# Kernel optimization log

Hardware: AMD Instinct MI355X
Metric: run time of the kernel (lower is better)

## Reference

```python
import jax, jax.numpy as jnp
import numpy as np

IMG = 1280
STRIDES = (8, 16, 32)
ALPHA, GAMMA = 0.25, 2.0
OBJ_W, BOX_W, FOOT_W = 1.0, 5.0, 1.0
RADIUS, NUM_CAND, EPS = 2.5, 10, 1e-7


def _grid(H, W):
    ys, xs = jnp.meshgrid(jnp.arange(H, dtype=jnp.float32),
                          jnp.arange(W, dtype=jnp.float32), indexing='ij')
    return xs.reshape(-1), ys.reshape(-1)


def _iou_xyxy(a, b):
    lt = jnp.maximum(a[..., :2], b[..., :2])
    rb = jnp.minimum(a[..., 2:], b[..., 2:])
    wh = jnp.clip(rb - lt, 0.0)
    inter = wh[..., 0] * wh[..., 1]
    aa = (a[..., 2] - a[..., 0]) * (a[..., 3] - a[..., 1])
    ab = (b[..., 2] - b[..., 0]) * (b[..., 3] - b[..., 1])
    return inter / (aa + ab - inter + EPS)


def _assign_one(pred, gt_boxes, gt_foots, gt_valid, stride):
    # Faithful SimOTAAssigner.assign for one image/scale (torch @no_grad).
    pred = jax.lax.stop_gradient(pred)
    gt_boxes = jax.lax.stop_gradient(gt_boxes)
    gt_foots = jax.lax.stop_gradient(gt_foots)
    C, H, W = pred.shape
    HW = H * W
    gx, gy = _grid(H, W)
    s = stride / IMG
    p = pred.reshape(C, HW)
    obj_logit = p[0]
    pcx = (jax.nn.sigmoid(p[1]) + gx) * s
    pcy = (jax.nn.sigmoid(p[2]) + gy) * s
    pw = jnp.exp(jnp.clip(p[3], -5.0, 5.0)) * s
    ph = jnp.exp(jnp.clip(p[4], -5.0, 5.0)) * s
    pred_xyxy = jnp.stack([pcx - pw / 2, pcy - ph / 2, pcx + pw / 2, pcy + ph / 2], -1)
    cls_cost = jax.nn.softplus(-obj_logit)  # BCE_with_logits(logit, 1)
    cell = jnp.arange(HW)

    def step(carry, gt):
        obj_t, box_t, foot_t, pos_m = carry
        box, foot, valid = gt
        cx, cy, w, h = box[0], box[1], box[2], box[3]
        cxg, cyg = cx / s, cy / s
        in_center = (jnp.abs(gx - cxg) < RADIUS) & (jnp.abs(gy - cyg) < RADIUS)
        in_box = ((gx >= (cx - w / 2) / s) & (gx < (cx + w / 2) / s) &
                  (gy >= (cy - h / 2) / s) & (gy < (cy + h / 2) / s))
        cand = in_center | in_box
        dist = (gx - cxg) ** 2 + (gy - cyg) ** 2
        cand = jnp.where(jnp.any(cand), cand, cell == jnp.argmin(dist))
        gt_xyxy = jnp.stack([cx - w / 2, cy - h / 2, cx + w / 2, cy + h / 2])
        iou = _iou_xyxy(pred_xyxy, gt_xyxy)  # (HW,)
        cost = jnp.where(cand, cls_cost - 3.0 * jnp.log(iou + EPS), jnp.inf)
        n_cand = jnp.sum(cand)
        iou_sum = jnp.sum(jnp.where(cand, iou, 0.0))
        n_pos = jnp.clip(jnp.floor(iou_sum).astype(jnp.int32), 1,
                         jnp.minimum(NUM_CAND, n_cand))
        _, idx = jax.lax.top_k(-cost, NUM_CAND)
        sel = (jnp.arange(NUM_CAND) < n_pos) & valid
        best_iou = iou[idx[0]]  # pair_iou[topk_idx[0]] in the torch code
        pos_m = pos_m.at[idx].max(sel.astype(jnp.float32))
        obj_t = obj_t.at[idx].max(jnp.where(sel, best_iou, -jnp.inf))
        tx = cxg - gx[idx]
        ty = cyg - gy[idx]
        tw = jnp.log(w / s + EPS)
        th = jnp.log(h / s + EPS)
        new_box = jnp.stack([tx, ty, jnp.full_like(tx, tw), jnp.full_like(tx, th)], 0)
        box_t = box_t.at[:, idx].set(jnp.where(sel, new_box, box_t[:, idx]))
        new_foot = jnp.stack([jnp.full_like(tx, foot[0]), jnp.full_like(tx, foot[1])], 0)
        foot_t = foot_t.at[:, idx].set(jnp.where(sel, new_foot, foot_t[:, idx]))
        return (obj_t, box_t, foot_t, pos_m), None

    init = (jnp.zeros(HW), jnp.zeros((4, HW)), jnp.zeros((2, HW)), jnp.zeros(HW))
    (obj_t, box_t, foot_t, pos_m), _ = jax.lax.scan(
        step, init, (gt_boxes, gt_foots, gt_valid))
    return obj_t, box_t, foot_t, pos_m


def _ciou(pcx, pcy, pw, ph, tcx, tcy, tw, th):
    px1, py1, px2, py2 = pcx - pw / 2, pcy - ph / 2, pcx + pw / 2, pcy + ph / 2
    tx1, ty1, tx2, ty2 = tcx - tw / 2, tcy - th / 2, tcx + tw / 2, tcy + th / 2
    iw = jnp.clip(jnp.minimum(px2, tx2) - jnp.maximum(px1, tx1), 0.0)
    ih = jnp.clip(jnp.minimum(py2, ty2) - jnp.maximum(py1, ty1), 0.0)
    inter = iw * ih
    union = pw * ph + tw * th - inter + EPS
    iou = inter / union
    rho2 = (pcx - tcx) ** 2 + (pcy - tcy) ** 2
    cw = jnp.maximum(px2, tx2) - jnp.minimum(px1, tx1)
    ch = jnp.maximum(py2, ty2) - jnp.minimum(py1, ty1)
    c2 = cw ** 2 + ch ** 2 + EPS
    v = (4.0 / jnp.pi ** 2) * (jnp.arctan(tw / (th + EPS)) - jnp.arctan(pw / (ph + EPS))) ** 2
    alpha = jax.lax.stop_gradient(v / (1.0 - iou + v + EPS))
    return iou - rho2 / c2 - alpha * v


def _loss_one(pred, gt_boxes, gt_foots, gt_valid, stride):
    obj_t, box_t, foot_t, pm = _assign_one(pred, gt_boxes, gt_foots, gt_valid, stride)
    C, H, W = pred.shape
    HW = H * W
    p = pred.reshape(C, HW)
    gx, gy = _grid(H, W)
    s = stride / IMG
    # focal loss on objectness with soft IoU targets
    x, z = p[0], obj_t
    ce = jnp.maximum(x, 0.0) - x * z + jnp.log1p(jnp.exp(-jnp.abs(x)))
    prob = jax.nn.sigmoid(x)
    p_t = prob * z + (1.0 - prob) * (1.0 - z)
    a_t = ALPHA * z + (1.0 - ALPHA) * (1.0 - z)
    obj_loss = jnp.mean(a_t * (1.0 - p_t) ** GAMMA * ce)
    npos = jnp.maximum(jnp.sum(pm), 1.0)
    # CIoU box loss at positive cells (mask instead of gather, jit-friendly)
    pcx = (jax.nn.sigmoid(p[1]) + gx) * s
    pcy = (jax.nn.sigmoid(p[2]) + gy) * s
    pw = jnp.exp(jnp.clip(p[3], -5.0, 5.0)) * s
    ph = jnp.exp(jnp.clip(p[4], -5.0, 5.0)) * s
    tcx = (box_t[0] + gx) * s
    tcy = (box_t[1] + gy) * s
    tw = jnp.exp(box_t[2]) * s
    th = jnp.exp(box_t[3]) * s
    ciou = _ciou(pcx, pcy, pw, ph, tcx, tcy, tw, th)
    box_loss = jnp.sum(pm * (1.0 - ciou)) / npos
    # smooth-L1 foot loss on sigmoid-decoded foot point
    pf = jax.nn.sigmoid(p[5:7])
    d = jnp.abs(pf - foot_t)
    sl1 = jnp.where(d < 1.0, 0.5 * d * d, d - 0.5)
    foot_loss = jnp.sum(pm * jnp.sum(sl1, 0)) / npos
    return obj_loss, box_loss, foot_loss


def _forward(pred_s0, pred_s1, pred_s2, targets):
    B = pred_s0.shape[0]
    person = targets[..., 0] == 0  # person_mask; padded rows use cls != 0
    boxes = targets[..., 1:5]
    foots = targets[..., 5:7]
    size = jnp.maximum(boxes[..., 2], boxes[..., 3]) * IMG
    scale_masks = (size < 128.0, (size >= 48.0) & (size < 288.0), size >= 128.0)
    tot_obj = tot_box = tot_foot = 0.0
    for pred, stride, sm in zip((pred_s0, pred_s1, pred_s2), STRIDES, scale_masks):
        valid = person & sm
        o, bx, f = jax.vmap(_loss_one, in_axes=(0, 0, 0, 0, None))(
            pred, boxes, foots, valid, stride)
        tot_obj = tot_obj + jnp.sum(o)
        tot_box = tot_box + jnp.sum(bx)
        tot_foot = tot_foot + jnp.sum(f)
    return (OBJ_W * tot_obj + BOX_W * tot_box + FOOT_W * tot_foot) / B


def setup_inputs() -> dict:
    key = jax.random.key(0)
    ks = jax.random.split(key, 7)
    B, N = 64, 40
    pred_s0 = jax.random.normal(ks[0], (B, 7, 160, 160), jnp.float32)
    pred_s1 = jax.random.normal(ks[1], (B, 7, 80, 80), jnp.float32)
    pred_s2 = jax.random.normal(ks[2], (B, 7, 40, 40), jnp.float32)
    cls = (jax.random.uniform(ks[3], (B, N, 1)) > 0.9).astype(jnp.float32)
    cxy = jax.random.uniform(ks[4], (B, N, 2)) * 0.8 + 0.1
    wh = jax.random.uniform(ks[5], (B, N, 2)) * 0.28 + 0.01
    ft = jax.random.uniform(ks[6], (B, N, 2))
    targets = jnp.concatenate([cls, cxy, wh, ft], -1)
    return {"pred_s0": pred_s0, "pred_s1": pred_s1, "pred_s2": pred_s2,
            "targets": targets}


def reference(pred_s0, pred_s1, pred_s2, targets):
    return _forward(pred_s0, pred_s1, pred_s2, targets)
```

## Files before the change

kernel.cpp:

```cpp
#include <hip/hip_runtime.h>
#include <math.h>

#define NBATCH 64
#define NGT    40
#define HW0    25600
#define HW1    6400
#define HW2    1600
#define NTASK  (NBATCH*3*NGT)
#define MAXE   400
#define SENT   0xFFFFFFFFFFFFFFFFull
#define FEPS   1e-7f

__device__ __forceinline__ float frcp(float x){ return __builtin_amdgcn_rcpf(x); }
__device__ __forceinline__ float fsigm(float x){ return frcp(1.0f + __expf(-x)); }
__device__ __forceinline__ float sigm(float x){ return 1.0f/(1.0f+expf(-x)); }

__device__ __forceinline__ float focal0(float x){
  float e = __expf(-fabsf(x));
  float ce = fmaxf(x,0.0f) + __logf(1.0f+e);
  float prob = fsigm(x);
  return 0.75f*prob*prob*ce;
}
__device__ __forceinline__ float focalz(float x, float z){
  float e = __expf(-fabsf(x));
  float ce = fmaxf(x,0.0f) - x*z + __logf(1.0f+e);
  float prob = fsigm(x);
  float p_t = prob*z + (1.0f-prob)*(1.0f-z);
  float a_t = 0.25f*z + 0.75f*(1.0f-z);
  float om = 1.0f-p_t;
  return a_t*om*om*ce;
}

__device__ __forceinline__ unsigned fkey(float f){
  unsigned b = __float_as_uint(f);
  return (b & 0x80000000u) ? ~b : (b | 0x80000000u);
}

__device__ __forceinline__ unsigned long long shflx64(unsigned long long v, int m){
  int lo = __shfl_xor((int)(unsigned)(v & 0xFFFFFFFFull), m, 64);
  int hi = __shfl_xor((int)(unsigned)(v >> 32), m, 64);
  return (((unsigned long long)(unsigned)hi) << 32) | (unsigned)lo;
}
__device__ __forceinline__ float wredf(float v){
  #pragma unroll
  for (int o=32;o;o>>=1) v += __shfl_xor(v,o,64);
  return v;
}
__device__ __forceinline__ int wredi(int v){
  #pragma unroll
  for (int o=32;o;o>>=1) v += __shfl_xor(v,o,64);
  return v;
}
__device__ __forceinline__ unsigned long long wredmin64(unsigned long long v){
  #pragma unroll
  for (int o=32;o;o>>=1){ unsigned long long w = shflx64(v,o); v = (w<v)?w:v; }
  return v;
}

__device__ __forceinline__ float iou_of_cell(const float* __restrict__ P, int HW, int cell,
                                             int W, float s,
                                             float bx1, float by1, float bx2, float by2, float ab){
  int gy = cell / W;
  int gx = cell - gy*W;
  float gxf=(float)gx, gyf=(float)gy;
  float q1 = P[HW+cell], q2=P[2*HW+cell], q3=P[3*HW+cell], q4=P[4*HW+cell];
  float pcx = (sigm(q1)+gxf)*s;
  float pcy = (sigm(q2)+gyf)*s;
  float pw = expf(fminf(fmaxf(q3,-5.0f),5.0f))*s;
  float ph = expf(fminf(fmaxf(q4,-5.0f),5.0f))*s;
  float ax1=pcx-pw*0.5f, ay1=pcy-ph*0.5f, ax2=pcx+pw*0.5f, ay2=pcy+ph*0.5f;
  float ltx=fmaxf(ax1,bx1), lty=fmaxf(ay1,by1);
  float rbx=fminf(ax2,bx2), rby=fminf(ay2,by2);
  float iw=fmaxf(rbx-ltx,0.0f), ih=fmaxf(rby-lty,0.0f);
  float inter=iw*ih;
  float aa=(ax2-ax1)*(ay2-ay1);
  return inter/(aa+ab-inter+FEPS);
}

__global__ __launch_bounds__(256) void k_assign(
    const float* __restrict__ p0, const float* __restrict__ p1,
    const float* __restrict__ p2, const float* __restrict__ tg,
    int2* __restrict__ meta, int* __restrict__ cells,
    float* __restrict__ out)
{
  if (blockIdx.x == 0 && threadIdx.x == 0) out[0] = 0.0f;
  int lane = threadIdx.x & 63;
  int task = ((blockIdx.x<<8) + threadIdx.x) >> 6;
  int g  = task % NGT;
  int bs = task / NGT;
  int sc = bs % 3;
  int b  = bs / 3;

  const float* tp = tg + (b*NGT + g)*7;
  float cls = tp[0], cx = tp[1], cy = tp[2], w = tp[3], h = tp[4];
  float sz = fmaxf(w,h)*1280.0f;
  bool valid = (cls == 0.0f);
  if (sc==0)      valid = valid && (sz < 128.0f);
  else if (sc==1) valid = valid && (sz >= 48.0f) && (sz < 288.0f);
  else            valid = valid && (sz >= 128.0f);
  if (!valid){ if (lane==0) meta[task] = make_int2(0,0); return; }

  int W, HW; float s; const float* P;
  if (sc==0)      { W=160; HW=HW0; s=8.0f/1280.0f;  P=p0; }
  else if (sc==1) { W=80;  HW=HW1; s=16.0f/1280.0f; P=p1; }
  else            { W=40;  HW=HW2; s=32.0f/1280.0f; P=p2; }
  P += (size_t)b*7*HW;

  float inv_s = 1280.0f/(float)((sc==0)?8:(sc==1)?16:32);
  float cxg = cx*inv_s, cyg = cy*inv_s;
  float bx1 = cx - w*0.5f, bx2 = cx + w*0.5f;
  float by1 = cy - h*0.5f, by2 = cy + h*0.5f;
  float ab  = (bx2-bx1)*(by2-by1);
  float bxl = bx1*inv_s, bxr = bx2*inv_s, byt = by1*inv_s, byb = by2*inv_s;

  int x0 = max(0,   (int)floorf(fminf(cxg-2.5f, bxl)) - 1);
  int x1 = min(W-1, (int)floorf(fmaxf(cxg+2.5f, bxr)) + 1);
  int y0 = max(0,   (int)floorf(fminf(cyg-2.5f, byt)) - 1);
  int y1 = min(W-1, (int)floorf(fmaxf(cyg+2.5f, byb)) + 1);
  int rw = x1-x0+1, rh = y1-y0+1;
  int rn = rw*rh;

  unsigned long long t[10];
  #pragma unroll
  for (int j=0;j<10;++j) t[j]=SENT;
  int ncand = 0; float iousum = 0.0f;
  unsigned long long dmin = SENT;

  int rx = lane % rw, ry = lane / rw;
  int stepy = 64 / rw, stepx = 64 % rw;
  for (int r = lane; r < rn; r += 64){
    float gxf = (float)(x0+rx), gyf = (float)(y0+ry);
    int cell = (y0+ry)*W + (x0+rx);
    float q1 = P[HW+cell], q2 = P[2*HW+cell], q3 = P[3*HW+cell], q4 = P[4*HW+cell];
    float pcx = (fsigm(q1)+gxf)*s;
    float pcy = (fsigm(q2)+gyf)*s;
    float pw = __expf(fminf(fmaxf(q3,-5.0f),5.0f))*s;
    float ph = __expf(fminf(fmaxf(q4,-5.0f),5.0f))*s;
    float ax1 = pcx-pw*0.5f, ay1 = pcy-ph*0.5f, ax2 = pcx+pw*0.5f, ay2 = pcy+ph*0.5f;
    float ltx = fmaxf(ax1,bx1), lty = fmaxf(ay1,by1);
    float rbx = fminf(ax2,bx2), rby = fminf(ay2,by2);
    float iw = fmaxf(rbx-ltx,0.0f), ih = fmaxf(rby-lty,0.0f);
    float inter = iw*ih;
    float aa = (ax2-ax1)*(ay2-ay1);
    float iou = inter * frcp(aa+ab-inter+FEPS);
    bool ic = (fabsf(gxf-cxg)<2.5f) && (fabsf(gyf-cyg)<2.5f);
    bool ib = (gxf>=bxl)&&(gxf<bxr)&&(gyf>=byt)&&(gyf<byb);
    float dx = gxf-cxg, dy = gyf-cyg;
    float dist = dx*dx+dy*dy;
    unsigned long long dk = (((unsigned long long)__float_as_uint(dist))<<32)|(unsigned)cell;
    dmin = (dk<dmin)?dk:dmin;
    if (ic|ib){
      ncand += 1; iousum += iou;
      float q0 = P[cell];
      float ccost = fmaxf(-q0,0.0f) + __logf(1.0f + __expf(-fabsf(q0)));
      float cost = ccost - 3.0f*__logf(iou+FEPS);
      unsigned long long pk = (((unsigned long long)fkey(cost))<<32)|(unsigned)cell;
      if (pk < t[9]){
        t[9] = pk;
        #pragma unroll
        for (int j=9;j>0;--j){ if (t[j]<t[j-1]){ unsigned long long tmp=t[j]; t[j]=t[j-1]; t[j-1]=tmp; } }
      }
    }
    rx += stepx; ry += stepy;
    if (rx >= rw){ rx -= rw; ry += 1; }
  }

  int NC = wredi(ncand);
  float IS = wredf(iousum);
  dmin = wredmin64(dmin);

  unsigned long long g10[10];
  int ptr = 0;
  #pragma unroll
  for (int rd=0; rd<10; ++rd){
    unsigned long long head = SENT;
    #pragma unroll
    for (int j=0;j<10;++j) head = (ptr==j)? t[j] : head;
    unsigned long long m = wredmin64(head);
    g10[rd] = m;
    if (head==m && m!=SENT) ptr += 1;
  }

  if (lane==0){
    unsigned cell0; int npos;
    if (NC==0){ cell0 = (unsigned)dmin; npos = 1; }
    else {
      cell0 = (unsigned)g10[0];
      int ub = NC < 10 ? NC : 10;
      int v = (int)floorf(IS);
      v = v < 1 ? 1 : v;
      npos = v > ub ? ub : v;
    }
    float biou = iou_of_cell(P, HW, (int)cell0, W, s, bx1, by1, bx2, by2, ab);
    meta[task] = make_int2(npos, __float_as_int(biou));
    #pragma unroll
    for (int sl=0; sl<10; ++sl){
      if (sl < npos) cells[task*10 + sl] = (int)((sl==0)? cell0 : (unsigned)g10[sl]);
    }
  }
}

__global__ __launch_bounds__(512) void k_pos(
    const float* __restrict__ p0, const float* __restrict__ p1,
    const float* __restrict__ p2, const float* __restrict__ tg,
    const int2* __restrict__ meta, const int* __restrict__ cells,
    float* __restrict__ out)
{
  __shared__ int   s_pack[MAXE];
  __shared__ float s_biou[MAXE];
  __shared__ int   s_cnt;
  __shared__ float red[4][8];

  int u = blockIdx.x;
  int b = u / 3, sc = u - b*3;
  int W, HW; float s; const float* P;
  if (sc==0)      { W=160; HW=HW0; s=8.0f/1280.0f;  P=p0; }
  else if (sc==1) { W=80;  HW=HW1; s=16.0f/1280.0f; P=p1; }
  else            { W=40;  HW=HW2; s=32.0f/1280.0f; P=p2; }
  P += (size_t)b*7*HW;

  if (threadIdx.x == 0) s_cnt = 0;
  __syncthreads();

  int tbase = (b*3 + sc)*NGT;
  if (threadIdx.x < NGT*10){
    int g = threadIdx.x / 10, sl = threadIdx.x - g*10;
    int2 m = meta[tbase + g];
    if (sl < m.x){
      int idx = atomicAdd(&s_cnt, 1);
      s_pack[idx] = (cells[(tbase+g)*10 + sl] << 6) | g;
      s_biou[idx] = __int_as_float(m.y);
    }
  }
  __syncthreads();
  int E = s_cnt;

  float osum = 0.0f, np = 0.0f, bsum = 0.0f, fsum = 0.0f;

  const float4* P4 = (const float4*)P;
  int n4 = HW >> 2;
  for (int i = threadIdx.x; i < n4; i += 512){
    float4 x4 = P4[i];
    osum += focal0(x4.x) + focal0(x4.y) + focal0(x4.z) + focal0(x4.w);
  }

  if (threadIdx.x < E){
    int myp = s_pack[threadIdx.x];
    int mycell = myp >> 6;
    int pm = myp; float bm = s_biou[threadIdx.x];
    for (int j = 0; j < E; ++j){
      int p = s_pack[j];
      if ((p>>6) == mycell){
        pm = max(pm, p);
        bm = fmaxf(bm, s_biou[j]);
      }
    }
    if (pm == myp){
      np = 1.0f;
      int wg = myp & 63;
      float z = bm;
      int i = mycell;
      float x = P[i];
      osum += focalz(x, z) - focal0(x);
      const float* tpb = tg + (b*NGT + wg)*7;
      float cx=tpb[1], cy=tpb[2], w=tpb[3], h=tpb[4], fx=tpb[5], fy=tpb[6];
      int gyi = i / W;
      float gxf = (float)(i - gyi*W), gyf = (float)gyi;
      float pcx = (fsigm(P[HW+i])+gxf)*s;
      float pcy = (fsigm(P[2*HW+i])+gyf)*s;
      float pw = __expf(fminf(fmaxf(P[3*HW+i],-5.0f),5.0f))*s;
      float ph = __expf(fminf(fmaxf(P[4*HW+i],-5.0f),5.0f))*s;
      float tw = w + FEPS*s, th = h + FEPS*s;
      float px1=pcx-pw*0.5f, py1=pcy-ph*0.5f, px2=pcx+pw*0.5f, py2=pcy+ph*0.5f;
      float tx1=cx-tw*0.5f, ty1=cy-th*0.5f, tx2=cx+tw*0.5f, ty2=cy+th*0.5f;
      float iw = fmaxf(fminf(px2,tx2)-fmaxf(px1,tx1),0.0f);
      float ih = fmaxf(fminf(py2,ty2)-fmaxf(py1,ty1),0.0f);
      float inter = iw*ih;
      float uni = pw*ph + tw*th - inter + FEPS;
      float iou = inter/uni;
      float rho2 = (pcx-cx)*(pcx-cx)+(pcy-cy)*(pcy-cy);
      float cw = fmaxf(px2,tx2)-fminf(px1,tx1);
      float ch = fmaxf(py2,ty2)-fminf(py1,ty1);
      float c2 = cw*cw+ch*ch+FEPS;
      float da = atanf(tw/(th+FEPS)) - atanf(pw/(ph+FEPS));
      float v = (4.0f/(float)(M_PI*M_PI))*da*da;
      float alpha = v/(1.0f-iou+v+FEPS);
      float ciou = iou - rho2/c2 - alpha*v;
      bsum = 1.0f - ciou;
      float pf1 = fsigm(P[5*HW+i]);
      float pf2 = fsigm(P[6*HW+i]);
      float d1 = fabsf(pf1-fx), d2 = fabsf(pf2-fy);
      fsum = (d1<1.0f? 0.5f*d1*d1 : d1-0.5f) + (d2<1.0f? 0.5f*d2*d2 : d2-0.5f);
    }
  }

  int wv = threadIdx.x >> 6, lane = threadIdx.x & 63;
  osum = wredf(osum); np = wredf(np); bsum = wredf(bsum); fsum = wredf(fsum);
  if (lane==0){ red[0][wv]=osum; red[1][wv]=np; red[2][wv]=bsum; red[3][wv]=fsum; }
  __syncthreads();
  if (threadIdx.x==0){
    float a0=0,a1=0,a2=0,a3=0;
    #pragma unroll
    for (int j=0;j<8;++j){ a0+=red[0][j]; a1+=red[1][j]; a2+=red[2][j]; a3+=red[3][j]; }
    float hw = (float)HW;
    float npz = fmaxf(a1, 1.0f);
    float c = (a0/hw + 5.0f*a2/npz + a3/npz) * (1.0f/64.0f);
    atomicAdd(out, c);
  }
}

extern "C" void kernel_launch(void* const* d_in, const int* in_sizes, int n_in,
                              void* d_out, int out_size, void* d_ws, size_t ws_size,
                              hipStream_t stream) {
  (void)in_sizes; (void)n_in; (void)out_size; (void)ws_size;
  const float* p0 = (const float*)d_in[0];
  const float* p1 = (const float*)d_in[1];
  const float* p2 = (const float*)d_in[2];
  const float* tg = (const float*)d_in[3];

  int2*  meta  = (int2*)d_ws;
  int*   cells = (int*)((char*)d_ws + (size_t)NTASK*8);
  float* out   = (float*)d_out;

  k_assign<<<NTASK/4, 256, 0, stream>>>(p0, p1, p2, tg, meta, cells, out);
  k_pos   <<<NBATCH*3, 512, 0, stream>>>(p0, p1, p2, tg, meta, cells, out);
}
```

Baseline: 117.5 us.

## Fuse background focal sum into assign kernel and simplify SimOTA cost ranking

The per-image objectness focal-loss sum moves out of the 192-block k_pos kernel and into k_assign. Each of the 10 blocks that share an (image, scale) pair reduces one tenth of the objectness map and writes a partial sum to workspace. The SimOTA cost key is replaced by a monotone equivalent, (1+exp(-x))/(iou+eps)^3, which avoids the log and softplus calls. The top-k merge now runs only npos rounds instead of 10. The fast sigmoid, exp and reciprocal are also used for the final IoU. In exchange, k_assign does extra streaming work and invalid tasks no longer exit early.

```diff
diff --git a/kernel.cpp b/kernel.cpp
--- a/kernel.cpp
+++ b/kernel.cpp
@@ -7,13 +7,13 @@
 #define HW1    6400
 #define HW2    1600
 #define NTASK  (NBATCH*3*NGT)
+#define NABLK  (NTASK/4)
 #define MAXE   400
 #define SENT   0xFFFFFFFFFFFFFFFFull
 #define FEPS   1e-7f
 
 __device__ __forceinline__ float frcp(float x){ return __builtin_amdgcn_rcpf(x); }
 __device__ __forceinline__ float fsigm(float x){ return frcp(1.0f + __expf(-x)); }
-__device__ __forceinline__ float sigm(float x){ return 1.0f/(1.0f+expf(-x)); }
 
 __device__ __forceinline__ float focal0(float x){
   float e = __expf(-fabsf(x));
@@ -31,11 +31,6 @@
   return a_t*om*om*ce;
 }
 
-__device__ __forceinline__ unsigned fkey(float f){
-  unsigned b = __float_as_uint(f);
-  return (b & 0x80000000u) ? ~b : (b | 0x80000000u);
-}
-
 __device__ __forceinline__ unsigned long long shflx64(unsigned long long v, int m){
   int lo = __shfl_xor((int)(unsigned)(v & 0xFFFFFFFFull), m, 64);
   int hi = __shfl_xor((int)(unsigned)(v >> 32), m, 64);
@@ -57,35 +52,36 @@
   return v;
 }
 
-__device__ __forceinline__ float iou_of_cell(const float* __restrict__ P, int HW, int cell,
-                                             int W, float s,
-                                             float bx1, float by1, float bx2, float by2, float ab){
+__device__ __forceinline__ float iou_of_cell_f(const float* __restrict__ P, int HW, int cell,
+                                               int W, float s,
+                                               float bx1, float by1, float bx2, float by2, float ab){
   int gy = cell / W;
   int gx = cell - gy*W;
   float gxf=(float)gx, gyf=(float)gy;
   float q1 = P[HW+cell], q2=P[2*HW+cell], q3=P[3*HW+cell], q4=P[4*HW+cell];
-  float pcx = (sigm(q1)+gxf)*s;
-  float pcy = (sigm(q2)+gyf)*s;
-  float pw = expf(fminf(fmaxf(q3,-5.0f),5.0f))*s;
-  float ph = expf(fminf(fmaxf(q4,-5.0f),5.0f))*s;
+  float pcx = (fsigm(q1)+gxf)*s;
+  float pcy = (fsigm(q2)+gyf)*s;
+  float pw = __expf(fminf(fmaxf(q3,-5.0f),5.0f))*s;
+  float ph = __expf(fminf(fmaxf(q4,-5.0f),5.0f))*s;
   float ax1=pcx-pw*0.5f, ay1=pcy-ph*0.5f, ax2=pcx+pw*0.5f, ay2=pcy+ph*0.5f;
   float ltx=fmaxf(ax1,bx1), lty=fmaxf(ay1,by1);
   float rbx=fminf(ax2,bx2), rby=fminf(ay2,by2);
   float iw=fmaxf(rbx-ltx,0.0f), ih=fmaxf(rby-lty,0.0f);
   float inter=iw*ih;
   float aa=(ax2-ax1)*(ay2-ay1);
-  return inter/(aa+ab-inter+FEPS);
+  return inter*frcp(aa+ab-inter+FEPS);
 }
 
 __global__ __launch_bounds__(256) void k_assign(
     const float* __restrict__ p0, const float* __restrict__ p1,
     const float* __restrict__ p2, const float* __restrict__ tg,
     int2* __restrict__ meta, int* __restrict__ cells,
-    float* __restrict__ out)
+    float* __restrict__ ws_focal, float* __restrict__ out)
 {
   if (blockIdx.x == 0 && threadIdx.x == 0) out[0] = 0.0f;
   int lane = threadIdx.x & 63;
-  int task = ((blockIdx.x<<8) + threadIdx.x) >> 6;
+  int wv   = threadIdx.x >> 6;
+  int task = (blockIdx.x<<2) + wv;
   int g  = task % NGT;
   int bs = task / NGT;
   int sc = bs % 3;
@@ -98,7 +94,6 @@
   if (sc==0)      valid = valid && (sz < 128.0f);
   else if (sc==1) valid = valid && (sz >= 48.0f) && (sz < 288.0f);
   else            valid = valid && (sz >= 128.0f);
-  if (!valid){ if (lane==0) meta[task] = make_int2(0,0); return; }
 
   int W, HW; float s; const float* P;
   if (sc==0)      { W=160; HW=HW0; s=8.0f/1280.0f;  P=p0; }
@@ -106,105 +101,120 @@
   else            { W=40;  HW=HW2; s=32.0f/1280.0f; P=p2; }
   P += (size_t)b*7*HW;
 
-  float inv_s = 1280.0f/(float)((sc==0)?8:(sc==1)?16:32);
-  float cxg = cx*inv_s, cyg = cy*inv_s;
-  float bx1 = cx - w*0.5f, bx2 = cx + w*0.5f;
-  float by1 = cy - h*0.5f, by2 = cy + h*0.5f;
-  float ab  = (bx2-bx1)*(by2-by1);
-  float bxl = bx1*inv_s, bxr = bx2*inv_s, byt = by1*inv_s, byb = by2*inv_s;
-
-  int x0 = max(0,   (int)floorf(fminf(cxg-2.5f, bxl)) - 1);
-  int x1 = min(W-1, (int)floorf(fmaxf(cxg+2.5f, bxr)) + 1);
-  int y0 = max(0,   (int)floorf(fminf(cyg-2.5f, byt)) - 1);
-  int y1 = min(W-1, (int)floorf(fmaxf(cyg+2.5f, byb)) + 1);
-  int rw = x1-x0+1, rh = y1-y0+1;
-  int rn = rw*rh;
-
-  unsigned long long t[10];
-  #pragma unroll
-  for (int j=0;j<10;++j) t[j]=SENT;
-  int ncand = 0; float iousum = 0.0f;
-  unsigned long long dmin = SENT;
-
-  int rx = lane % rw, ry = lane / rw;
-  int stepy = 64 / rw, stepx = 64 % rw;
-  for (int r = lane; r < rn; r += 64){
-    float gxf = (float)(x0+rx), gyf = (float)(y0+ry);
-    int cell = (y0+ry)*W + (x0+rx);
-    float q1 = P[HW+cell], q2 = P[2*HW+cell], q3 = P[3*HW+cell], q4 = P[4*HW+cell];
-    float pcx = (fsigm(q1)+gxf)*s;
-    float pcy = (fsigm(q2)+gyf)*s;
-    float pw = __expf(fminf(fmaxf(q3,-5.0f),5.0f))*s;
-    float ph = __expf(fminf(fmaxf(q4,-5.0f),5.0f))*s;
-    float ax1 = pcx-pw*0.5f, ay1 = pcy-ph*0.5f, ax2 = pcx+pw*0.5f, ay2 = pcy+ph*0.5f;
-    float ltx = fmaxf(ax1,bx1), lty = fmaxf(ay1,by1);
-    float rbx = fminf(ax2,bx2), rby = fminf(ay2,by2);
-    float iw = fmaxf(rbx-ltx,0.0f), ih = fmaxf(rby-lty,0.0f);
-    float inter = iw*ih;
-    float aa = (ax2-ax1)*(ay2-ay1);
-    float iou = inter * frcp(aa+ab-inter+FEPS);
-    bool ic = (fabsf(gxf-cxg)<2.5f) && (fabsf(gyf-cyg)<2.5f);
-    bool ib = (gxf>=bxl)&&(gxf<bxr)&&(gyf>=byt)&&(gyf<byb);
-    float dx = gxf-cxg, dy = gyf-cyg;
-    float dist = dx*dx+dy*dy;
-    unsigned long long dk = (((unsigned long long)__float_as_uint(dist))<<32)|(unsigned)cell;
-    dmin = (dk<dmin)?dk:dmin;
-    if (ic|ib){
-      ncand += 1; iousum += iou;
-      float q0 = P[cell];
-      float ccost = fmaxf(-q0,0.0f) + __logf(1.0f + __expf(-fabsf(q0)));
-      float cost = ccost - 3.0f*__logf(iou+FEPS);
-      unsigned long long pk = (((unsigned long long)fkey(cost))<<32)|(unsigned)cell;
-      if (pk < t[9]){
-        t[9] = pk;
-        #pragma unroll
-        for (int j=9;j>0;--j){ if (t[j]<t[j-1]){ unsigned long long tmp=t[j]; t[j]=t[j-1]; t[j-1]=tmp; } }
+  if (!valid){
+    if (lane==0) meta[task] = make_int2(0,0);
+  } else {
+    float inv_s = 1280.0f/(float)((sc==0)?8:(sc==1)?16:32);
+    float cxg = cx*inv_s, cyg = cy*inv_s;
+    float bx1 = cx - w*0.5f, bx2 = cx + w*0.5f;
+    float by1 = cy - h*0.5f, by2 = cy + h*0.5f;
+    float ab  = (bx2-bx1)*(by2-by1);
+    float bxl = bx1*inv_s, bxr = bx2*inv_s, byt = by1*inv_s, byb = by2*inv_s;
+
+    int x0 = max(0,   (int)floorf(fminf(cxg-2.5f, bxl)) - 1);
+    int x1 = min(W-1, (int)floorf(fmaxf(cxg+2.5f, bxr)) + 1);
+    int y0 = max(0,   (int)floorf(fminf(cyg-2.5f, byt)) - 1);
+    int y1 = min(W-1, (int)floorf(fmaxf(cyg+2.5f, byb)) + 1);
+    int rw = x1-x0+1, rh = y1-y0+1;
+    int rn = rw*rh;
+
+    unsigned long long t[10];
+    #pragma unroll
+    for (int j=0;j<10;++j) t[j]=SENT;
+    int ncand = 0; float iousum = 0.0f;
+    unsigned long long dmin = SENT;
+
+    int rx = lane % rw, ry = lane / rw;
+    int stepy = 64 / rw, stepx = 64 % rw;
+    for (int r = lane; r < rn; r += 64){
+      float gxf = (float)(x0+rx), gyf = (float)(y0+ry);
+      int cell = (y0+ry)*W + (x0+rx);
+      float q1 = P[HW+cell], q2 = P[2*HW+cell], q3 = P[3*HW+cell], q4 = P[4*HW+cell];
+      float pcx = (fsigm(q1)+gxf)*s;
+      float pcy = (fsigm(q2)+gyf)*s;
+      float pw = __expf(fminf(fmaxf(q3,-5.0f),5.0f))*s;
+      float ph = __expf(fminf(fmaxf(q4,-5.0f),5.0f))*s;
+      float ax1 = pcx-pw*0.5f, ay1 = pcy-ph*0.5f, ax2 = pcx+pw*0.5f, ay2 = pcy+ph*0.5f;
+      float ltx = fmaxf(ax1,bx1), lty = fmaxf(ay1,by1);
+      float rbx = fminf(ax2,bx2), rby = fminf(ay2,by2);
+      float iw = fmaxf(rbx-ltx,0.0f), ih = fmaxf(rby-lty,0.0f);
+      float inter = iw*ih;
+      float aa = (ax2-ax1)*(ay2-ay1);
+      float iou = inter * frcp(aa+ab-inter+FEPS);
+      bool ic = (fabsf(gxf-cxg)<2.5f) && (fabsf(gyf-cyg)<2.5f);
+      bool ib = (gxf>=bxl)&&(gxf<bxr)&&(gyf>=byt)&&(gyf<byb);
+      float dx = gxf-cxg, dy = gyf-cyg;
+      float dist = dx*dx+dy*dy;
+      unsigned long long dk = (((unsigned long long)__float_as_uint(dist))<<32)|(unsigned)cell;
+      dmin = (dk<dmin)?dk:dmin;
+      if (ic|ib){
+        ncand += 1; iousum += iou;
+        float q0 = P[cell];
+        float ti = iou + FEPS;
+        float ratio = (1.0f + __expf(-q0)) * frcp(ti*ti*ti);
+        unsigned long long pk = (((unsigned long long)__float_as_uint(ratio))<<32)|(unsigned)cell;
+        if (pk < t[9]){
+          t[9] = pk;
+          #pragma unroll
+          for (int j=9;j>0;--j){ if (t[j]<t[j-1]){ unsigned long long tmp=t[j]; t[j]=t[j-1]; t[j-1]=tmp; } }
+        }
       }
-    }
-    rx += stepx; ry += stepy;
-    if (rx >= rw){ rx -= rw; ry += 1; }
-  }
-
-  int NC = wredi(ncand);
-  float IS = wredf(iousum);
-  dmin = wredmin64(dmin);
-
-  unsigned long long g10[10];
-  int ptr = 0;
-  #pragma unroll
-  for (int rd=0; rd<10; ++rd){
-    unsigned long long head = SENT;
-    #pragma unroll
-    for (int j=0;j<10;++j) head = (ptr==j)? t[j] : head;
-    unsigned long long m = wredmin64(head);
-    g10[rd] = m;
-    if (head==m && m!=SENT) ptr += 1;
-  }
-
-  if (lane==0){
-    unsigned cell0; int npos;
-    if (NC==0){ cell0 = (unsigned)dmin; npos = 1; }
-    else {
-      cell0 = (unsigned)g10[0];
+      rx += stepx; ry += stepy;
+      if (rx >= rw){ rx -= rw; ry += 1; }
+    }
+
+    int NC = wredi(ncand);
+    float IS = wredf(iousum);
+    dmin = wredmin64(dmin);
+
+    int npos, cell0;
+    if (NC==0){
+      npos = 1; cell0 = (int)(unsigned)dmin;
+      if (lane==0) cells[task*10] = cell0;
+    } else {
       int ub = NC < 10 ? NC : 10;
       int v = (int)floorf(IS);
       v = v < 1 ? 1 : v;
       npos = v > ub ? ub : v;
-    }
-    float biou = iou_of_cell(P, HW, (int)cell0, W, s, bx1, by1, bx2, by2, ab);
-    meta[task] = make_int2(npos, __float_as_int(biou));
-    #pragma unroll
-    for (int sl=0; sl<10; ++sl){
-      if (sl < npos) cells[task*10 + sl] = (int)((sl==0)? cell0 : (unsigned)g10[sl]);
-    }
-  }
+      int ptr = 0; cell0 = 0;
+      for (int rd=0; rd<npos; ++rd){
+        unsigned long long head = SENT;
+        #pragma unroll
+        for (int j=0;j<10;++j) head = (ptr==j)? t[j] : head;
+        unsigned long long m = wredmin64(head);
+        if (rd==0) cell0 = (int)(unsigned)m;
+        if (lane==0) cells[task*10+rd] = (int)(unsigned)m;
+        if (head==m && m!=SENT) ptr += 1;
+      }
+    }
+    if (lane==0){
+      float biou = iou_of_cell_f(P, HW, cell0, W, s, bx1, by1, bx2, by2, ab);
+      meta[task] = make_int2(npos, __float_as_int(biou));
+    }
+  }
+
+  float osum = 0.0f;
+  {
+    int chunk = blockIdx.x % 10;
+    int n4c = (HW/10) >> 2;
+    const float4* Q4 = (const float4*)P + chunk*n4c;
+    for (int i = threadIdx.x; i < n4c; i += 256){
+      float4 x4 = Q4[i];
+      osum += focal0(x4.x) + focal0(x4.y) + focal0(x4.z) + focal0(x4.w);
+    }
+  }
+  osum = wredf(osum);
+  __shared__ float redf[4];
+  if (lane==0) redf[wv] = osum;
+  __syncthreads();
+  if (threadIdx.x==0) ws_focal[blockIdx.x] = redf[0]+redf[1]+redf[2]+redf[3];
 }
 
 __global__ __launch_bounds__(512) void k_pos(
     const float* __restrict__ p0, const float* __restrict__ p1,
     const float* __restrict__ p2, const float* __restrict__ tg,
     const int2* __restrict__ meta, const int* __restrict__ cells,
-    float* __restrict__ out)
+    const float* __restrict__ ws_focal, float* __restrict__ out)
 {
   __shared__ int   s_pack[MAXE];
   __shared__ float s_biou[MAXE];
@@ -222,7 +232,7 @@
   if (threadIdx.x == 0) s_cnt = 0;
   __syncthreads();
 
-  int tbase = (b*3 + sc)*NGT;
+  int tbase = u*NGT;
   if (threadIdx.x < NGT*10){
     int g = threadIdx.x / 10, sl = threadIdx.x - g*10;
     int2 m = meta[tbase + g];
@@ -237,12 +247,7 @@
 
   float osum = 0.0f, np = 0.0f, bsum = 0.0f, fsum = 0.0f;
 
-  const float4* P4 = (const float4*)P;
-  int n4 = HW >> 2;
-  for (int i = threadIdx.x; i < n4; i += 512){
-    float4 x4 = P4[i];
-    osum += focal0(x4.x) + focal0(x4.y) + focal0(x4.z) + focal0(x4.w);
-  }
+  if (threadIdx.x < 10) osum = ws_focal[u*10 + threadIdx.x];
 
   if (threadIdx.x < E){
     int myp = s_pack[threadIdx.x];
@@ -318,10 +323,11 @@
   const float* p2 = (const float*)d_in[2];
   const float* tg = (const float*)d_in[3];
 
-  int2*  meta  = (int2*)d_ws;
-  int*   cells = (int*)((char*)d_ws + (size_t)NTASK*8);
-  float* out   = (float*)d_out;
-
-  k_assign<<<NTASK/4, 256, 0, stream>>>(p0, p1, p2, tg, meta, cells, out);
-  k_pos   <<<NBATCH*3, 512, 0, stream>>>(p0, p1, p2, tg, meta, cells, out);
-}
+  int2*  meta     = (int2*)d_ws;
+  int*   cells    = (int*)((char*)d_ws + (size_t)NTASK*8);
+  float* ws_focal = (float*)((char*)d_ws + (size_t)NTASK*48);
+  float* out      = (float*)d_out;
+
+  k_assign<<<NABLK, 256, 0, stream>>>(p0, p1, p2, tg, meta, cells, ws_focal, out);
+  k_pos   <<<NBATCH*3, 512, 0, stream>>>(p0, p1, p2, tg, meta, cells, ws_focal, out);
+}
```

Measured after the change: 106.9 us (median of 2 runs). -9.0%, faster.
